# Performance work log

Hardware: AMD Instinct MI355X
Metric: run time of the kernel (lower is better)

The kernel has to match this reference:

```python
import jax, jax.numpy as jnp
import numpy as np

BOUND = 1.0
DENSITY_SCALE = 1.0
NUM_STEPS = 128
UPSAMPLE_STEPS = 128
MAX_FAR = 5.0
MIN_NEAR = 0.2


def setup_inputs() -> dict:
    key = jax.random.key(0)
    ks = jax.random.split(key, 10)
    N, H, G = 16384, 64, 15
    return {
        "rays_o": jax.random.normal(ks[0], (N, 3), jnp.float32) * 0.5,
        "rays_d": jax.random.normal(ks[1], (N, 3), jnp.float32),
        "W1": jax.random.normal(ks[2], (3, H), jnp.float32) * 0.5,
        "b1": jnp.zeros((H,), jnp.float32),
        "W2": jax.random.normal(ks[3], (H, 1 + G), jnp.float32) * 0.3,
        "b2": jnp.zeros((1 + G,), jnp.float32),
        "Wc1": jax.random.normal(ks[4], (3 + 3 + G, H), jnp.float32) * 0.3,
        "bc1": jnp.zeros((H,), jnp.float32),
        "Wc2": jax.random.normal(ks[5], (H, 3), jnp.float32) * 0.3,
        "bc2": jnp.zeros((3,), jnp.float32),
    }


def _density(x, W1, b1, W2, b2):
    # x: [P,3] -> sigma [P], geo_feat [P,G]
    h = jax.nn.relu(x @ W1 + b1)
    o = h @ W2 + b2
    return jax.nn.softplus(o[..., 0]), o[..., 1:]


def _color(x, d, geo, Wc1, bc1, Wc2, bc2):
    inp = jnp.concatenate([x, d, geo], axis=-1)
    h = jax.nn.relu(inp @ Wc1 + bc1)
    return jax.nn.sigmoid(h @ Wc2 + bc2)


def _near_far_from_aabb(o, d, lo, hi):
    ds = jnp.where(jnp.abs(d) < 1e-8, 1e-8, d)
    t1 = (lo - o) / ds
    t2 = (hi - o) / ds
    near = jnp.max(jnp.minimum(t1, t2), axis=-1)
    far = jnp.min(jnp.maximum(t1, t2), axis=-1)
    return near, far


def _composite(z_vals, sigma, sample_dist):
    # z_vals, sigma: [N,S]; sample_dist: [N,1]
    deltas = z_vals[..., 1:] - z_vals[..., :-1]
    deltas = jnp.concatenate([deltas, sample_dist * jnp.ones_like(deltas[..., :1])], axis=-1)
    alphas = 1.0 - jnp.exp(-deltas * DENSITY_SCALE * sigma)
    shifted = jnp.concatenate([jnp.ones_like(alphas[..., :1]), 1.0 - alphas + 1e-15], axis=-1)
    weights = alphas * jnp.cumprod(shifted, axis=-1)[..., :-1]
    return weights, deltas


def _sample_pdf(bins, weights, n_samples):
    # bins: [N,M+1], weights: [N,M]  (deterministic, det=True)
    weights = weights + 1e-5
    pdf = weights / jnp.sum(weights, axis=-1, keepdims=True)
    cdf = jnp.cumsum(pdf, axis=-1)
    cdf = jnp.concatenate([jnp.zeros_like(cdf[..., :1]), cdf], axis=-1)  # [N,M+1]
    M = cdf.shape[-1] - 1
    u = jnp.linspace(0.5 / n_samples, 1.0 - 0.5 / n_samples, n_samples, dtype=cdf.dtype)
    u = jnp.broadcast_to(u, cdf.shape[:-1] + (n_samples,))
    inds = jax.vmap(lambda c, uu: jnp.searchsorted(c, uu, side="right"))(cdf, u)
    below = jnp.maximum(inds - 1, 0)
    above = jnp.minimum(inds, M)
    cdf0 = jnp.take_along_axis(cdf, below, axis=-1)
    cdf1 = jnp.take_along_axis(cdf, above, axis=-1)
    b0 = jnp.take_along_axis(bins, below, axis=-1)
    b1 = jnp.take_along_axis(bins, above, axis=-1)
    denom = cdf1 - cdf0
    denom = jnp.where(denom < 1e-5, jnp.ones_like(denom), denom)
    t = (u - cdf0) / denom
    return b0 + t * (b1 - b0)


def reference(rays_o, rays_d, W1, b1, W2, b2, Wc1, bc1, Wc2, bc2):
    N = rays_o.shape[0]
    rays_d = rays_d / jnp.linalg.norm(rays_d, axis=-1, keepdims=True)
    lo = jnp.full((3,), -BOUND, rays_o.dtype)
    hi = jnp.full((3,), BOUND, rays_o.dtype)

    nears, fars = _near_far_from_aabb(rays_o, rays_d, lo, hi)
    fars = jnp.maximum(jnp.minimum(fars, MAX_FAR), MIN_NEAR)
    nears = jnp.minimum(jnp.maximum(nears, MIN_NEAR), MAX_FAR)
    nears = nears[:, None]
    fars = fars[:, None]

    z_vals = nears + (fars - nears) * jnp.linspace(0.0, 1.0, NUM_STEPS, dtype=rays_o.dtype)[None, :]
    sample_dist = (fars - nears) / NUM_STEPS  # [N,1]

    xyzs = rays_o[:, None, :] + rays_d[:, None, :] * z_vals[..., None]
    xyzs = jnp.clip(xyzs, lo, hi)
    sigma, geo = _density(xyzs.reshape(-1, 3), W1, b1, W2, b2)
    sigma = sigma.reshape(N, NUM_STEPS)
    geo = geo.reshape(N, NUM_STEPS, -1)

    # --- importance resampling (no_grad block in torch) ---
    w_c, deltas_c = _composite(z_vals, sigma, sample_dist)
    z_mid = z_vals[..., :-1] + 0.5 * deltas_c[..., :-1]
    new_z = _sample_pdf(z_mid, w_c[:, 1:-1], UPSAMPLE_STEPS)
    new_z = jax.lax.stop_gradient(new_z)
    new_xyzs = rays_o[:, None, :] + rays_d[:, None, :] * new_z[..., None]
    new_xyzs = jax.lax.stop_gradient(jnp.clip(new_xyzs, lo, hi))
    new_sigma, new_geo = _density(new_xyzs.reshape(-1, 3), W1, b1, W2, b2)
    new_sigma = new_sigma.reshape(N, UPSAMPLE_STEPS)
    new_geo = new_geo.reshape(N, UPSAMPLE_STEPS, -1)

    # merge + sort along sample axis
    z_all = jnp.concatenate([z_vals, new_z], axis=1)
    idx = jnp.argsort(z_all, axis=1)
    z_all = jnp.take_along_axis(z_all, idx, axis=1)
    xyz_all = jnp.take_along_axis(jnp.concatenate([xyzs, new_xyzs], axis=1), idx[..., None], axis=1)
    sigma_all = jnp.take_along_axis(jnp.concatenate([sigma, new_sigma], axis=1), idx, axis=1)
    geo_all = jnp.take_along_axis(jnp.concatenate([geo, new_geo], axis=1), idx[..., None], axis=1)

    weights, _ = _composite(z_all, sigma_all, sample_dist)
    S = z_all.shape[1]
    dirs = jnp.broadcast_to(rays_d[:, None, :], (N, S, 3))
    mask = weights > 1e-4
    rgb = _color(xyz_all.reshape(-1, 3), dirs.reshape(-1, 3), geo_all.reshape(-1, geo_all.shape[-1]), Wc1, bc1, Wc2, bc2)
    rgbs = jnp.where(mask.reshape(-1)[:, None], rgb, 0.0).reshape(N, S, 3)

    weights_sum = jnp.sum(weights, axis=-1)
    image = jnp.sum(weights[..., None] * rgbs, axis=-2)
    image = image + (1.0 - weights_sum)[..., None] * 1.0  # white bg
    return image
```

## Files before the change

kernel.cpp:

```cpp
#include <hip/hip_runtime.h>
#include <hip/hip_fp16.h>
#include <math.h>

#define NRAYS 16384
#define HID 64

typedef float    float4_ __attribute__((ext_vector_type(4)));
typedef _Float16 half8   __attribute__((ext_vector_type(8)));
typedef __fp16   fp16x2  __attribute__((ext_vector_type(2)));

__device__ __forceinline__ float clip1(float v){ return fminf(fmaxf(v,-1.f),1.f); }
__device__ __forceinline__ float softplusf_(float x){
  return fmaxf(x,0.f) + __logf(1.f + __expf(-fabsf(x)));
}
__device__ __forceinline__ float sigmoidf_(float x){
  return __fdividef(1.f, 1.f + __expf(-x));
}
__device__ __forceinline__ float h2f(unsigned short u){
  union { unsigned short s; __fp16 h; } cv; cv.s = u; return (float)cv.h;
}

__device__ __forceinline__ unsigned int pkh(float a, float b){
  union { fp16x2 h; unsigned int u; } cv;
  cv.h = __builtin_amdgcn_cvt_pkrtz(a, b);
  return cv.u;
}
__device__ __forceinline__ unsigned long long pk64(float4_ a){
  return (unsigned long long)pkh(a[0],a[1]) | ((unsigned long long)pkh(a[2],a[3])<<32);
}
__device__ __forceinline__ unsigned int relu_pk(unsigned int x){
  unsigned int y;
  __asm__("v_pk_max_f16 %0, %1, 0" : "=v"(y) : "v"(x));
  return y;
}

__device__ __forceinline__ void load_ray(const float* ro, const float* rd, int r,
    float& ox,float& oy,float& oz,float& dx,float& dy,float& dz){
  ox=ro[3*r]; oy=ro[3*r+1]; oz=ro[3*r+2];
  dx=rd[3*r]; dy=rd[3*r+1]; dz=rd[3*r+2];
  float inv = 1.f/sqrtf(dx*dx+dy*dy+dz*dz);
  dx*=inv; dy*=inv; dz*=inv;
}

__device__ __forceinline__ void aabb_nf(float ox,float oy,float oz,float dx,float dy,float dz,
    float& nears,float& fars){
  float dsx = (fabsf(dx)<1e-8f)?1e-8f:dx;
  float dsy = (fabsf(dy)<1e-8f)?1e-8f:dy;
  float dsz = (fabsf(dz)<1e-8f)?1e-8f:dz;
  float t1x=(-1.f-ox)/dsx, t2x=(1.f-ox)/dsx;
  float t1y=(-1.f-oy)/dsy, t2y=(1.f-oy)/dsy;
  float t1z=(-1.f-oz)/dsz, t2z=(1.f-oz)/dsz;
  float nr = fmaxf(fmaxf(fminf(t1x,t2x),fminf(t1y,t2y)),fminf(t1z,t2z));
  float fr = fminf(fminf(fmaxf(t1x,t2x),fmaxf(t1y,t2y)),fmaxf(t1z,t2z));
  fars  = fmaxf(fminf(fr,5.f),0.2f);
  nears = fminf(fmaxf(nr,0.2f),5.f);
}

__device__ __forceinline__ float wave_excl_chunk(float chunk, int lane, float& total){
  float incl = chunk;
  #pragma unroll
  for(int off=1; off<64; off<<=1){
    float n = __shfl_up(incl, off, 64);
    if (lane >= off) incl += n;
  }
  total = __shfl(incl, 63, 64);
  return incl - chunk;
}

__global__ void prep_weights(const float* __restrict__ W1, const float* __restrict__ W2,
                             const float* __restrict__ Wc1, const float* __restrict__ Wc2,
                             unsigned short* __restrict__ wb){
  int idx = blockIdx.x*256 + threadIdx.x;
  if (idx >= 6144) return;
  int f = idx>>3, j = idx&7, lane = f&63, slot = f>>6, q = lane>>4, c = lane&15;
  int k = q*8+j;
  float v = 0.f;
  if (slot < 4){        if (k<3) v = W1[k*HID + slot*16 + c]; }
  else if (slot < 6){   int h=(slot-4)*32+k; v = W2[h*16 + c]; }
  else if (slot < 10){  int mt=slot-6;
                        int row = (k==0)? -1 : (k<16 ? 5+k : (k<22 ? k-16 : -1));
                        if (row>=0) v = Wc1[row*HID + mt*16 + c]; }
  else {                int h=(slot-10)*32+k; if (c<3) v = Wc2[h*3 + c]; }
  wb[idx] = __half_as_ushort(__float2half_rn(v));
}

__device__ __forceinline__ void storeH(unsigned short* H, float4_ a, int t, int hbase){
  unsigned int lo = relu_pk(pkh(a[0],a[1]));
  unsigned int hi = relu_pk(pkh(a[2],a[3]));
  *(unsigned long long*)&H[hbase + t*256] =
      (unsigned long long)lo | ((unsigned long long)hi<<32);
}

__global__ __launch_bounds__(128) void nerf_fused(
    const float* __restrict__ ro, const float* __restrict__ rd,
    const float* __restrict__ b1, const float* __restrict__ b2,
    const float* __restrict__ bc1, const float* __restrict__ bc2,
    const unsigned short* __restrict__ wb, float* __restrict__ out)
{
  __shared__ __align__(16) unsigned short Hfrag[2][2][1024];
  __shared__ __align__(16) unsigned long long RGBS[2][256];
  __shared__ __align__(16) float zBs[2][128];

  const int tid = threadIdx.x, lane = tid&63, wv = tid>>6;
  const int q = lane>>4, c = lane&15;
  const int r = blockIdx.x*2 + wv;

  float ox,oy,oz,dx,dy,dz;
  load_ray(ro,rd,r,ox,oy,oz,dx,dy,dz);
  float nears,fars; aabb_nf(ox,oy,oz,dx,dy,dz,nears,fars);
  const float step  = (fars-nears)*(1.f/127.f);
  const float sdist = (fars-nears)*(1.f/128.f);
  const bool asc = (nears <= fars);
  const unsigned int pk_dydz = pkh(dy,dz);

  const half8* WF = (const half8*)wb;
  half8 aW1T[4], aW2T[2], aWc1T[4], aWc2T[2];
  #pragma unroll
  for(int t=0;t<4;t++){ aW1T[t] = WF[t*64+lane]; aWc1T[t] = WF[(6+t)*64+lane]; }
  #pragma unroll
  for(int k=0;k<2;k++){ aW2T[k] = WF[(4+k)*64+lane]; aWc2T[k] = WF[(10+k)*64+lane]; }
  float4_ b1v[4], bc1v[4];
  #pragma unroll
  for(int t=0;t<4;t++){
    b1v[t]  = *(const float4_*)&b1[t*16+q*4];
    bc1v[t] = *(const float4_*)&bc1[t*16+q*4];
  }
  const float4_ bTd = *(const float4_*)&b2[q*4];
  float4_ bTc = (float4_){0.f,0.f,0.f,0.f};
  if (q==0){ bTc[0]=bc2[0]; bTc[1]=bc2[1]; bTc[2]=bc2[2]; }

  unsigned short* H0 = &Hfrag[wv][0][0];
  unsigned short* H1 = &Hfrag[wv][1][0];
  unsigned long long* RGBSw = RGBS[wv];
  float* zBsw = zBs[wv];
  float* cdfw = (float*)&Hfrag[wv][0][0];
  float* zMw  = (float*)&Hfrag[wv][0][0];
  const int hbase  = (q>>1)*128 + c*8 + (q&1)*4;
  const int lread  = lane*8;
  const int ba0 = (q*32 + c)*4;
  const int ba1 = ba0 + 64;

  auto pairbody = [&](int p, int sbase, bool coarse){
    const int sidx0 = p*32 + c, sidx1 = p*32 + 16 + c;
    half8 bf0 = (half8)(_Float16)0, bf1 = (half8)(_Float16)0;
    unsigned int c0a=0u,c0b=0u,c1a=0u,c1b=0u;
    if ((q&1)==0){
      float z0 = coarse ? fmaf(step,(float)sidx0,nears) : zBsw[sidx0];
      float z1 = coarse ? fmaf(step,(float)sidx1,nears) : zBsw[sidx1];
      float x0 = clip1(fmaf(dx,z0,ox)), y0 = clip1(fmaf(dy,z0,oy)), g0 = clip1(fmaf(dz,z0,oz));
      float x1 = clip1(fmaf(dx,z1,ox)), y1 = clip1(fmaf(dy,z1,oy)), g1 = clip1(fmaf(dz,z1,oz));
      if (q==0){
        unsigned int* u0p = (unsigned int*)&bf0;
        u0p[0] = pkh(x0,y0); u0p[1] = pkh(g0,0.f);
        unsigned int* u1p = (unsigned int*)&bf1;
        u1p[0] = pkh(x1,y1); u1p[1] = pkh(g1,0.f);
      } else {
        c0a = pkh(x0,y0); c0b = pkh(g0,dx);
        c1a = pkh(x1,y1); c1b = pkh(g1,dx);
      }
    }
    #pragma unroll
    for(int t=0;t<4;t++){
      float4_ a0 = __builtin_amdgcn_mfma_f32_16x16x32_f16(aW1T[t], bf0, b1v[t], 0,0,0);
      float4_ a1 = __builtin_amdgcn_mfma_f32_16x16x32_f16(aW1T[t], bf1, b1v[t], 0,0,0);
      storeH(H0, a0, t, hbase);
      storeH(H1, a1, t, hbase);
    }
    half8 h00 = *(const half8*)&H0[lread];
    half8 h01 = *(const half8*)&H0[512 + lread];
    half8 h10 = *(const half8*)&H1[lread];
    half8 h11 = *(const half8*)&H1[512 + lread];
    float4_ o0 = __builtin_amdgcn_mfma_f32_16x16x32_f16(aW2T[0], h00, bTd, 0,0,0);
    o0 = __builtin_amdgcn_mfma_f32_16x16x32_f16(aW2T[1], h01, o0, 0,0,0);
    float4_ o1 = __builtin_amdgcn_mfma_f32_16x16x32_f16(aW2T[0], h10, bTd, 0,0,0);
    o1 = __builtin_amdgcn_mfma_f32_16x16x32_f16(aW2T[1], h11, o1, 0,0,0);
    unsigned int pg0a = pkh(o0[0],o0[1]), pg0b = pkh(o0[2],o0[3]);
    unsigned int pg1a = pkh(o1[0],o1[1]), pg1b = pkh(o1[2],o1[3]);
    half8 bcf0, bcf1;
    {
      unsigned int* u0p = (unsigned int*)&bcf0;
      unsigned int* u1p = (unsigned int*)&bcf1;
      u0p[0] = (unsigned int)__builtin_amdgcn_ds_bpermute(ba0, (int)pg0a);
      u0p[1] = (unsigned int)__builtin_amdgcn_ds_bpermute(ba0, (int)pg0b);
      u0p[2] = (unsigned int)__builtin_amdgcn_ds_bpermute(ba1, (int)pg0a);
      u0p[3] = (unsigned int)__builtin_amdgcn_ds_bpermute(ba1, (int)pg0b);
      u1p[0] = (unsigned int)__builtin_amdgcn_ds_bpermute(ba0, (int)pg1a);
      u1p[1] = (unsigned int)__builtin_amdgcn_ds_bpermute(ba0, (int)pg1b);
      u1p[2] = (unsigned int)__builtin_amdgcn_ds_bpermute(ba1, (int)pg1a);
      u1p[3] = (unsigned int)__builtin_amdgcn_ds_bpermute(ba1, (int)pg1b);
      if (q == 2){
        u0p[0] = c0a; u0p[1] = c0b; u0p[2] = pk_dydz; u0p[3] = 0u;
        u1p[0] = c1a; u1p[1] = c1b; u1p[2] = pk_dydz; u1p[3] = 0u;
      }
    }
    #pragma unroll
    for(int t=0;t<4;t++){
      float4_ a0 = __builtin_amdgcn_mfma_f32_16x16x32_f16(aWc1T[t], bcf0, bc1v[t], 0,0,0);
      float4_ a1 = __builtin_amdgcn_mfma_f32_16x16x32_f16(aWc1T[t], bcf1, bc1v[t], 0,0,0);
      storeH(H0, a0, t, hbase);
      storeH(H1, a1, t, hbase);
    }
    h00 = *(const half8*)&H0[lread];
    h01 = *(const half8*)&H0[512 + lread];
    h10 = *(const half8*)&H1[lread];
    h11 = *(const half8*)&H1[512 + lread];
    float4_ oc0 = __builtin_amdgcn_mfma_f32_16x16x32_f16(aWc2T[0], h00, bTc, 0,0,0);
    oc0 = __builtin_amdgcn_mfma_f32_16x16x32_f16(aWc2T[1], h01, oc0, 0,0,0);
    float4_ oc1 = __builtin_amdgcn_mfma_f32_16x16x32_f16(aWc2T[0], h10, bTc, 0,0,0);
    oc1 = __builtin_amdgcn_mfma_f32_16x16x32_f16(aWc2T[1], h11, oc1, 0,0,0);
    if (q==0){
      RGBSw[sbase+sidx0] = pk64((float4_){oc0[0], oc0[1], oc0[2], o0[0]});
      RGBSw[sbase+sidx1] = pk64((float4_){oc1[0], oc1[1], oc1[2], o1[0]});
    }
  };

  #pragma unroll
  for(int p=0;p<4;p++) pairbody(p, 0, true);

  {
    unsigned long long e0u = RGBSw[2*lane];
    unsigned long long e1u = RGBSw[2*lane+1];
    float s0 = softplusf_(h2f((unsigned short)(e0u>>48)));
    float s1 = softplusf_(h2f((unsigned short)(e1u>>48)));
    float d0 = (2*lane   < 127) ? step*s0 : 0.f;
    float d1 = (2*lane+1 < 127) ? step*s1 : 0.f;
    float tot;
    float e0 = wave_excl_chunk(d0+d1, lane, tot);
    float w0 = (1.f-__expf(-d0))*__expf(-e0);
    float w1 = (1.f-__expf(-d1))*__expf(-(e0+d0));
    float ww0 = (lane>=1 && 2*lane<127) ? w0+1e-5f : 0.f;
    float ww1 = (2*lane+1 < 127) ? w1+1e-5f : 0.f;
    float wsum;
    float ce0 = wave_excl_chunk(ww0+ww1, lane, wsum);
    float inv = __fdividef(1.f, wsum);
    cdfw[2*lane]   = (ce0+ww0)*inv;
    cdfw[2*lane+1] = (ce0+ww0+ww1)*inv;
  }

  {
    const float u0c = 0.5f/128.f;
    const float du = (1.f - 1.f/128.f)/127.f;
    #pragma unroll
    for(int j=0;j<2;j++){
      int k = lane + j*64;
      float u = fmaf(du,(float)k,u0c);
      int lo=0, hi=127;
      while(lo<hi){ int m=(lo+hi)>>1; if (cdfw[m] <= u) lo=m+1; else hi=m; }
      int below = max(lo-1,0), above = min(lo,126);
      float c0 = cdfw[below], c1 = cdfw[above];
      float bb0 = nears + step*((float)below + 0.5f);
      float bb1 = nears + step*((float)above + 0.5f);
      float den = c1 - c0; if (den < 1e-5f) den = 1.f;
      float zf = bb0 + (u - c0)/den*(bb1 - bb0);
      zBsw[asc ? k : 127-k] = zf;
    }
  }

  #pragma unroll
  for(int p=0;p<4;p++) pairbody(p, 128, false);

  #pragma unroll
  for(int j=0;j<2;j++){
    int sA = lane + j*64;
    int i = asc ? sA : 127-sA;
    float myz = fmaf(step,(float)i,nears);
    int lo=0, hi=128;
    while(lo<hi){ int m=(lo+hi)>>1; if (zBsw[m] < myz) lo=m+1; else hi=m; }
    int pos = sA + lo;
    zMw[pos] = __uint_as_float((__float_as_uint(myz) & ~255u) | (unsigned)i);
  }
  const float inv_step = (step != 0.f) ? __fdividef(1.f, step) : 0.f;
  #pragma unroll
  for(int j=0;j<2;j++){
    int k = lane + j*64;
    float myz = zBsw[k];
    float tt = (myz - nears)*inv_step;
    float mr = (step == 0.f) ? 200.f : (asc ? tt : 127.f - tt);
    mr = fminf(fmaxf(mr, -2.f), 130.f);
    int lo = (int)floorf(mr) + 1;
    lo = min(max(lo,0),128);
    while (lo<128 && fmaf(step,(float)(asc?lo:127-lo),nears) <= myz) lo++;
    while (lo>0  && fmaf(step,(float)(asc?(lo-1):(128-lo)),nears) >  myz) lo--;
    int pos = k + lo;
    zMw[pos] = __uint_as_float((__float_as_uint(myz) & ~255u) | (unsigned)(128+k));
  }

  float accR=0.f, accG=0.f, accB=0.f, accW=0.f;
  {
    float4_ z4 = *(const float4_*)&zMw[4*lane];
    float z5 = zMw[4*lane+4];
    int oi0 = (int)(__float_as_uint(z4[0]) & 255u);
    int oi1 = (int)(__float_as_uint(z4[1]) & 255u);
    int oi2 = (int)(__float_as_uint(z4[2]) & 255u);
    int oi3 = (int)(__float_as_uint(z4[3]) & 255u);
    unsigned long long p0 = RGBSw[oi0];
    unsigned long long p1 = RGBSw[oi1];
    unsigned long long p2 = RGBSw[oi2];
    unsigned long long p3 = RGBSw[oi3];
    float sg0 = softplusf_(h2f((unsigned short)(p0>>48)));
    float sg1 = softplusf_(h2f((unsigned short)(p1>>48)));
    float sg2 = softplusf_(h2f((unsigned short)(p2>>48)));
    float sg3 = softplusf_(h2f((unsigned short)(p3>>48)));
    float d0 = (z4[1]-z4[0])*sg0;
    float d1 = (z4[2]-z4[1])*sg1;
    float d2 = (z4[3]-z4[2])*sg2;
    float dl = (lane==63) ? sdist : (z5 - z4[3]);
    float d3 = dl*sg3;
    float tot;
    float S = wave_excl_chunk(d0+d1+d2+d3, lane, tot);
    float4_ w4;
    w4[0] = (1.f-__expf(-d0))*__expf(-S); S += d0;
    w4[1] = (1.f-__expf(-d1))*__expf(-S); S += d1;
    w4[2] = (1.f-__expf(-d2))*__expf(-S); S += d2;
    w4[3] = (1.f-__expf(-d3))*__expf(-S);
    accW = w4[0]+w4[1]+w4[2]+w4[3];
    if (w4[0] > 1e-4f){
      accR = fmaf(w4[0], sigmoidf_(h2f((unsigned short) p0      )), accR);
      accG = fmaf(w4[0], sigmoidf_(h2f((unsigned short)(p0>>16))), accG);
      accB = fmaf(w4[0], sigmoidf_(h2f((unsigned short)(p0>>32))), accB);
    }
    if (w4[1] > 1e-4f){
      accR = fmaf(w4[1], sigmoidf_(h2f((unsigned short) p1      )), accR);
      accG = fmaf(w4[1], sigmoidf_(h2f((unsigned short)(p1>>16))), accG);
      accB = fmaf(w4[1], sigmoidf_(h2f((unsigned short)(p1>>32))), accB);
    }
    if (w4[2] > 1e-4f){
      accR = fmaf(w4[2], sigmoidf_(h2f((unsigned short) p2      )), accR);
      accG = fmaf(w4[2], sigmoidf_(h2f((unsigned short)(p2>>16))), accG);
      accB = fmaf(w4[2], sigmoidf_(h2f((unsigned short)(p2>>32))), accB);
    }
    if (w4[3] > 1e-4f){
      accR = fmaf(w4[3], sigmoidf_(h2f((unsigned short) p3      )), accR);
      accG = fmaf(w4[3], sigmoidf_(h2f((unsigned short)(p3>>16))), accG);
      accB = fmaf(w4[3], sigmoidf_(h2f((unsigned short)(p3>>32))), accB);
    }
  }

  #pragma unroll
  for(int off=32; off; off>>=1){
    accR += __shfl_down(accR, off, 64);
    accG += __shfl_down(accG, off, 64);
    accB += __shfl_down(accB, off, 64);
    accW += __shfl_down(accW, off, 64);
  }
  if (lane == 0){
    float bg = 1.f - accW;
    out[r*3+0] = accR + bg;
    out[r*3+1] = accG + bg;
    out[r*3+2] = accB + bg;
  }
}

extern "C" void kernel_launch(void* const* d_in, const int* in_sizes, int n_in,
                              void* d_out, int out_size, void* d_ws, size_t ws_size,
                              hipStream_t stream) {
  const float* ro  = (const float*)d_in[0];
  const float* rd  = (const float*)d_in[1];
  const float* W1  = (const float*)d_in[2];
  const float* b1  = (const float*)d_in[3];
  const float* W2  = (const float*)d_in[4];
  const float* b2  = (const float*)d_in[5];
  const float* Wc1 = (const float*)d_in[6];
  const float* bc1 = (const float*)d_in[7];
  const float* Wc2 = (const float*)d_in[8];
  const float* bc2 = (const float*)d_in[9];
  float* out = (float*)d_out;

  unsigned short* wb = (unsigned short*)d_ws;

  prep_weights<<<dim3(24), dim3(256), 0, stream>>>(W1, W2, Wc1, Wc2, wb);
  nerf_fused<<<dim3(NRAYS/2), dim3(128), 0, stream>>>(
      ro, rd, b1, b2, bc1, bc2, wb, out);
}
```

Measured before the change: 172.8 us.

## Replace per-lane binary searches with LDS histogram and prefix-sum rank computation

Two per-lane binary searches are replaced with histogram counting: one inverts the CDF for importance sampling, the other finds merge positions between coarse and fine samples. Each CDF entry or fine z directly computes its bucket, atomically increments a shared histogram, and a wave prefix scan yields each query's rank. This removes divergent log-depth LDS search loops in favour of LDS atomics plus a scan. It adds atomic contention, extra LDS round trips, and relies on exact tie semantics matching the previous searches.

```diff
diff --git a/kernel.cpp b/kernel.cpp
--- a/kernel.cpp
+++ b/kernel.cpp
@@ -135,6 +135,8 @@
   float* zBsw = zBs[wv];
   float* cdfw = (float*)&Hfrag[wv][0][0];
   float* zMw  = (float*)&Hfrag[wv][0][0];
+  unsigned int* histw = (unsigned int*)&Hfrag[wv][1][0];
+  float* Hprew = (float*)&Hfrag[wv][1][512];
   const int hbase  = (q>>1)*128 + c*8 + (q&1)*4;
   const int lread  = lane*8;
   const int ba0 = (q*32 + c)*4;
@@ -217,6 +219,7 @@
   #pragma unroll
   for(int p=0;p<4;p++) pairbody(p, 0, true);
 
+  float cdfv0, cdfv1;
   {
     unsigned long long e0u = RGBSw[2*lane];
     unsigned long long e1u = RGBSw[2*lane+1];
@@ -233,19 +236,45 @@
     float wsum;
     float ce0 = wave_excl_chunk(ww0+ww1, lane, wsum);
     float inv = __fdividef(1.f, wsum);
-    cdfw[2*lane]   = (ce0+ww0)*inv;
-    cdfw[2*lane+1] = (ce0+ww0+ww1)*inv;
+    cdfv0 = (ce0+ww0)*inv;
+    cdfv1 = (ce0+ww0+ww1)*inv;
+    cdfw[2*lane]   = cdfv0;
+    cdfw[2*lane+1] = cdfv1;
   }
 
   {
     const float u0c = 0.5f/128.f;
     const float du = (1.f - 1.f/128.f)/127.f;
+    const float inv_du = 1.f/du;
+    histw[2*lane] = 0u; histw[2*lane+1] = 0u;
+    int km0, km1;
+    {
+      float kf = fminf(fmaxf((cdfv0 - u0c)*inv_du, 0.f), 128.f);
+      int k0 = (int)kf;
+      while (k0 < 128 && fmaf(du,(float)k0,u0c) < cdfv0) k0++;
+      while (k0 > 0   && fmaf(du,(float)(k0-1),u0c) >= cdfv0) k0--;
+      km0 = k0;
+    }
+    {
+      float kf = fminf(fmaxf((cdfv1 - u0c)*inv_du, 0.f), 128.f);
+      int k0 = (int)kf;
+      while (k0 < 128 && fmaf(du,(float)k0,u0c) < cdfv1) k0++;
+      while (k0 > 0   && fmaf(du,(float)(k0-1),u0c) >= cdfv1) k0--;
+      km1 = k0;
+    }
+    if (km0 < 128) atomicAdd(&histw[km0], 1u);
+    if (lane != 63 && km1 < 128) atomicAdd(&histw[km1], 1u);
+    float hb0 = (float)histw[2*lane];
+    float hb1 = (float)histw[2*lane+1];
+    float tot;
+    float ex = wave_excl_chunk(hb0+hb1, lane, tot);
+    Hprew[2*lane]   = ex + hb0;
+    Hprew[2*lane+1] = ex + hb0 + hb1;
     #pragma unroll
     for(int j=0;j<2;j++){
       int k = lane + j*64;
       float u = fmaf(du,(float)k,u0c);
-      int lo=0, hi=127;
-      while(lo<hi){ int m=(lo+hi)>>1; if (cdfw[m] <= u) lo=m+1; else hi=m; }
+      int lo = (int)Hprew[k];
       int below = max(lo-1,0), above = min(lo,126);
       float c0 = cdfw[below], c1 = cdfw[above];
       float bb0 = nears + step*((float)below + 0.5f);
@@ -259,30 +288,45 @@
   #pragma unroll
   for(int p=0;p<4;p++) pairbody(p, 128, false);
 
-  #pragma unroll
-  for(int j=0;j<2;j++){
-    int sA = lane + j*64;
-    int i = asc ? sA : 127-sA;
-    float myz = fmaf(step,(float)i,nears);
-    int lo=0, hi=128;
-    while(lo<hi){ int m=(lo+hi)>>1; if (zBsw[m] < myz) lo=m+1; else hi=m; }
-    int pos = sA + lo;
-    zMw[pos] = __uint_as_float((__float_as_uint(myz) & ~255u) | (unsigned)i);
-  }
-  const float inv_step = (step != 0.f) ? __fdividef(1.f, step) : 0.f;
-  #pragma unroll
-  for(int j=0;j<2;j++){
-    int k = lane + j*64;
-    float myz = zBsw[k];
-    float tt = (myz - nears)*inv_step;
-    float mr = (step == 0.f) ? 200.f : (asc ? tt : 127.f - tt);
-    mr = fminf(fmaxf(mr, -2.f), 130.f);
-    int lo = (int)floorf(mr) + 1;
-    lo = min(max(lo,0),128);
-    while (lo<128 && fmaf(step,(float)(asc?lo:127-lo),nears) <= myz) lo++;
-    while (lo>0  && fmaf(step,(float)(asc?(lo-1):(128-lo)),nears) >  myz) lo--;
-    int pos = k + lo;
-    zMw[pos] = __uint_as_float((__float_as_uint(myz) & ~255u) | (unsigned)(128+k));
+  {
+    const float inv_step = (step != 0.f) ? __fdividef(1.f, step) : 0.f;
+    int mk0, mk1;
+    #pragma unroll
+    for(int j=0;j<2;j++){
+      int k = lane + j*64;
+      float myz = zBsw[k];
+      float tt = (myz - nears)*inv_step;
+      float mr = (step == 0.f) ? 200.f : (asc ? tt : 127.f - tt);
+      mr = fminf(fmaxf(mr, -2.f), 130.f);
+      int lo = (int)floorf(mr) + 1;
+      lo = min(max(lo,0),128);
+      while (lo<128 && fmaf(step,(float)(asc?lo:127-lo),nears) <= myz) lo++;
+      while (lo>0  && fmaf(step,(float)(asc?(lo-1):(128-lo)),nears) >  myz) lo--;
+      if (j==0) mk0 = lo; else mk1 = lo;
+    }
+    histw[2*lane] = 0u; histw[2*lane+1] = 0u;
+    if (mk0 < 128) atomicAdd(&histw[mk0], 1u);
+    if (mk1 < 128) atomicAdd(&histw[mk1], 1u);
+    float hb0 = (float)histw[2*lane];
+    float hb1 = (float)histw[2*lane+1];
+    float tot;
+    float ex = wave_excl_chunk(hb0+hb1, lane, tot);
+    Hprew[2*lane]   = ex + hb0;
+    Hprew[2*lane+1] = ex + hb0 + hb1;
+    #pragma unroll
+    for(int j=0;j<2;j++){
+      int sA = lane + j*64;
+      int i = asc ? sA : 127-sA;
+      float myz = fmaf(step,(float)i,nears);
+      int pos = sA + (int)Hprew[sA];
+      zMw[pos] = __uint_as_float((__float_as_uint(myz) & ~255u) | (unsigned)i);
+    }
+    {
+      float z0 = zBsw[lane];
+      float z1 = zBsw[lane+64];
+      zMw[lane + mk0]      = __uint_as_float((__float_as_uint(z0) & ~255u) | (unsigned)(128+lane));
+      zMw[lane + 64 + mk1] = __uint_as_float((__float_as_uint(z1) & ~255u) | (unsigned)(192+lane));
+    }
   }
 
   float accR=0.f, accG=0.f, accB=0.f, accW=0.f;
```

Result: no change. 175.1 us (+1.3%).

## Compute first MLP layer analytically per ray when samples stay unclipped

Applied to the files above, without the earlier changes.

When the whole ray segment between near and far lies inside the unit box, clipping never fires. The first-layer pre-activation is then affine in z, so each lane precomputes per-ray base and slope terms for its hidden units and builds the hidden fragments directly with FMAs plus ReLU. This skips the first-layer MFMAs and the LDS store/reload round trip for those rays. Rays that clip fall back to the old MFMA path, which adds a divergent branch and extra registers for the per-ray coefficient arrays.

```diff
diff --git a/kernel.cpp b/kernel.cpp
--- a/kernel.cpp
+++ b/kernel.cpp
@@ -93,7 +93,8 @@
 
 __global__ __launch_bounds__(128) void nerf_fused(
     const float* __restrict__ ro, const float* __restrict__ rd,
-    const float* __restrict__ b1, const float* __restrict__ b2,
+    const float* __restrict__ W1g, const float* __restrict__ b1,
+    const float* __restrict__ b2,
     const float* __restrict__ bc1, const float* __restrict__ bc2,
     const unsigned short* __restrict__ wb, float* __restrict__ out)
 {
@@ -112,6 +113,29 @@
   const float sdist = (fars-nears)*(1.f/128.f);
   const bool asc = (nears <= fars);
   const unsigned int pk_dydz = pkh(dy,dz);
+
+  bool fastL1;
+  {
+    float xn = fmaf(dx,nears,ox), yn = fmaf(dy,nears,oy), zn = fmaf(dz,nears,oz);
+    float xf = fmaf(dx,fars,ox),  yf = fmaf(dy,fars,oy),  zf = fmaf(dz,fars,oz);
+    float mx = fmaxf(fmaxf(fmaxf(fabsf(xn),fabsf(yn)),fabsf(zn)),
+                     fmaxf(fmaxf(fabsf(xf),fabsf(yf)),fabsf(zf)));
+    fastL1 = (mx <= 1.0f);
+  }
+  float hbA[8], hdA[8], hbB[8], hdB[8];
+  {
+    const int r0 = q*8;
+    #pragma unroll
+    for(int j=0;j<8;j++){
+      int ra = r0 + j, rb = 32 + r0 + j;
+      float wa0=W1g[ra], wa1=W1g[64+ra], wa2=W1g[128+ra];
+      float wb0=W1g[rb], wb1=W1g[64+rb], wb2=W1g[128+rb];
+      hbA[j] = ox*wa0 + oy*wa1 + oz*wa2 + b1[ra];
+      hdA[j] = dx*wa0 + dy*wa1 + dz*wa2;
+      hbB[j] = ox*wb0 + oy*wb1 + oz*wb2 + b1[rb];
+      hdB[j] = dx*wb0 + dy*wb1 + dz*wb2;
+    }
+  }
 
   const half8* WF = (const half8*)wb;
   half8 aW1T[4], aW2T[2], aWc1T[4], aWc2T[2];
@@ -140,15 +164,36 @@
   const int ba0 = (q*32 + c)*4;
   const int ba1 = ba0 + 64;
 
+  auto mk8A = [&](float z)->half8 {
+    half8 h;
+    unsigned int* up = (unsigned int*)&h;
+    #pragma unroll
+    for(int j=0;j<4;j++)
+      up[j] = pkh(fmaxf(fmaf(z,hdA[2*j],hbA[2*j]),0.f),
+                  fmaxf(fmaf(z,hdA[2*j+1],hbA[2*j+1]),0.f));
+    return h;
+  };
+  auto mk8B = [&](float z)->half8 {
+    half8 h;
+    unsigned int* up = (unsigned int*)&h;
+    #pragma unroll
+    for(int j=0;j<4;j++)
+      up[j] = pkh(fmaxf(fmaf(z,hdB[2*j],hbB[2*j]),0.f),
+                  fmaxf(fmaf(z,hdB[2*j+1],hbB[2*j+1]),0.f));
+    return h;
+  };
+
   auto pairbody = [&](int p, int sbase, bool coarse){
     const int sidx0 = p*32 + c, sidx1 = p*32 + 16 + c;
+    float z0u, z1u;
+    if (coarse){ z0u = fmaf(step,(float)sidx0,nears); z1u = fmaf(step,(float)sidx1,nears); }
+    else       { z0u = zBsw[sidx0];                   z1u = zBsw[sidx1]; }
+
     half8 bf0 = (half8)(_Float16)0, bf1 = (half8)(_Float16)0;
     unsigned int c0a=0u,c0b=0u,c1a=0u,c1b=0u;
     if ((q&1)==0){
-      float z0 = coarse ? fmaf(step,(float)sidx0,nears) : zBsw[sidx0];
-      float z1 = coarse ? fmaf(step,(float)sidx1,nears) : zBsw[sidx1];
-      float x0 = clip1(fmaf(dx,z0,ox)), y0 = clip1(fmaf(dy,z0,oy)), g0 = clip1(fmaf(dz,z0,oz));
-      float x1 = clip1(fmaf(dx,z1,ox)), y1 = clip1(fmaf(dy,z1,oy)), g1 = clip1(fmaf(dz,z1,oz));
+      float x0 = clip1(fmaf(dx,z0u,ox)), y0 = clip1(fmaf(dy,z0u,oy)), g0 = clip1(fmaf(dz,z0u,oz));
+      float x1 = clip1(fmaf(dx,z1u,ox)), y1 = clip1(fmaf(dy,z1u,oy)), g1 = clip1(fmaf(dz,z1u,oz));
       if (q==0){
         unsigned int* u0p = (unsigned int*)&bf0;
         u0p[0] = pkh(x0,y0); u0p[1] = pkh(g0,0.f);
@@ -159,17 +204,23 @@
         c1a = pkh(x1,y1); c1b = pkh(g1,dx);
       }
     }
-    #pragma unroll
-    for(int t=0;t<4;t++){
-      float4_ a0 = __builtin_amdgcn_mfma_f32_16x16x32_f16(aW1T[t], bf0, b1v[t], 0,0,0);
-      float4_ a1 = __builtin_amdgcn_mfma_f32_16x16x32_f16(aW1T[t], bf1, b1v[t], 0,0,0);
-      storeH(H0, a0, t, hbase);
-      storeH(H1, a1, t, hbase);
-    }
-    half8 h00 = *(const half8*)&H0[lread];
-    half8 h01 = *(const half8*)&H0[512 + lread];
-    half8 h10 = *(const half8*)&H1[lread];
-    half8 h11 = *(const half8*)&H1[512 + lread];
+    half8 h00, h01, h10, h11;
+    if (fastL1){
+      h00 = mk8A(z0u); h01 = mk8B(z0u);
+      h10 = mk8A(z1u); h11 = mk8B(z1u);
+    } else {
+      #pragma unroll
+      for(int t=0;t<4;t++){
+        float4_ a0 = __builtin_amdgcn_mfma_f32_16x16x32_f16(aW1T[t], bf0, b1v[t], 0,0,0);
+        float4_ a1 = __builtin_amdgcn_mfma_f32_16x16x32_f16(aW1T[t], bf1, b1v[t], 0,0,0);
+        storeH(H0, a0, t, hbase);
+        storeH(H1, a1, t, hbase);
+      }
+      h00 = *(const half8*)&H0[lread];
+      h01 = *(const half8*)&H0[512 + lread];
+      h10 = *(const half8*)&H1[lread];
+      h11 = *(const half8*)&H1[512 + lread];
+    }
     float4_ o0 = __builtin_amdgcn_mfma_f32_16x16x32_f16(aW2T[0], h00, bTd, 0,0,0);
     o0 = __builtin_amdgcn_mfma_f32_16x16x32_f16(aW2T[1], h01, o0, 0,0,0);
     float4_ o1 = __builtin_amdgcn_mfma_f32_16x16x32_f16(aW2T[0], h10, bTd, 0,0,0);
@@ -370,5 +421,5 @@
 
   prep_weights<<<dim3(24), dim3(256), 0, stream>>>(W1, W2, Wc1, Wc2, wb);
   nerf_fused<<<dim3(NRAYS/2), dim3(128), 0, stream>>>(
-      ro, rd, b1, b2, bc1, bc2, wb, out);
-}
+      ro, rd, W1, b1, b2, bc1, bc2, wb, out);
+}
```

Measured after the change: 194.5 us. +12.6%, slower.
